# Optimization experiments

Hardware: AMD Instinct MI355X
Metric: run time of the kernel (lower is better)

Reference implementation:

```python
import jax, jax.numpy as jnp
import numpy as np

B, F, M, N, H, O = 8, 128, 256, 1024, 64, 128
BN_EPS = 1e-5
COS_EPS = 1e-8


def _bn(x, g, b, m, v):
    # inference-mode BatchNorm over channel axis 1
    shape = [1] * x.ndim
    shape[1] = -1
    return g.reshape(shape) * (x - m.reshape(shape)) * jax.lax.rsqrt(v.reshape(shape) + BN_EPS) + b.reshape(shape)


def setup_inputs() -> dict:
    key = jax.random.key(0)
    ks = jax.random.split(key, 24)
    def n(k, shape, s=1.0):
        return jax.random.normal(k, shape, dtype=jnp.float32) * s
    inp = {}
    inp['template_feature'] = n(ks[0], (B, F, M))
    inp['search_feature'] = n(ks[1], (B, F, N))
    # SharedMLP 1x1 conv weights (bias=False because bn=True)
    inp['W1'] = n(ks[2], (H, F + 1), 0.05)
    inp['W2'] = n(ks[3], (H, H), 0.05)
    inp['W3'] = n(ks[4], (H, H), 0.05)
    # fea_layer: conv1d(H, bn=True) then conv1d(O, activation=None, bias=True)
    inp['Wc1'] = n(ks[5], (H, H), 0.05)
    inp['Wc2'] = n(ks[6], (O, H), 0.05)
    inp['bc2'] = n(ks[7], (O,), 0.05)
    for i, nm in enumerate(['1', '2', '3', 'c1']):
        inp['g' + nm] = 1.0 + n(ks[8 + i], (H,), 0.1)
        inp['b' + nm] = n(ks[12 + i], (H,), 0.1)
        inp['m' + nm] = n(ks[16 + i], (H,), 0.01)
        inp['v' + nm] = jax.random.uniform(ks[20 + i], (H,), minval=0.5, maxval=1.5, dtype=jnp.float32)
    return inp


def reference(template_feature, search_feature, W1, W2, W3, Wc1, Wc2, bc2,
              g1, b1, m1, v1, g2, b2, m2, v2, g3, b3, m3, v3, gc1, bc1, mc1, vc1):
    t, s = template_feature, search_feature
    # pairwise cosine similarity over channel dim (no BxFxMxN expand needed)
    dot = jnp.einsum('bfm,bfn->bmn', t, s)
    nt = jnp.linalg.norm(t, axis=1)  # (B, M)
    ns = jnp.linalg.norm(s, axis=1)  # (B, N)
    cos = dot / jnp.maximum(nt[:, :, None] * ns[:, None, :], COS_EPS)  # (B, M, N)
    # first 1x1 conv on concat(cos, expand(t)) computed fused (no concat materialization)
    h = jnp.einsum('hf,bfm->bhm', W1[:, 1:], t)[..., None] + W1[:, 0][None, :, None, None] * cos[:, None]
    h = jax.nn.relu(_bn(h, g1, b1, m1, v1))  # (B, H, M, N)
    h = jax.nn.relu(_bn(jnp.einsum('gh,bhmn->bgmn', W2, h), g2, b2, m2, v2))
    h = jax.nn.relu(_bn(jnp.einsum('gh,bhmn->bgmn', W3, h), g3, b3, m3, v3))
    p = jnp.max(h, axis=2)  # max-pool over M -> (B, H, N)
    c = jax.nn.relu(_bn(jnp.einsum('gh,bhn->bgn', Wc1, p), gc1, bc1, mc1, vc1))
    return jnp.einsum('oh,bhn->bon', Wc2, c) + bc2[None, :, None]  # (B, O, N)
```

## Files before the change

### kernel.cpp

```cpp
#include <hip/hip_runtime.h>


#define BB 8
#define FF 128
#define MM 256
#define NN 1024
#define HH 64
#define OO 128
#define BN_EPS 1e-5f
#define COS_EPS 1e-8f

#define WS_U     0
#define WS_C2    64
#define WS_C3    128
#define WS_CC1   192
#define WS_W2F   256
#define WS_W3F   4352
#define WS_WC1F  8448
#define WS_A1    12544
#define WS_NT    143616
#define WS_NS    145664
#define WS_COSH  153856
#define WS_P     1202432
#define PS       524288

typedef _Float16 half2v __attribute__((ext_vector_type(2)));
typedef _Float16 half8  __attribute__((ext_vector_type(8)));
typedef __attribute__((ext_vector_type(4))) float f32x4;

__device__ __forceinline__ unsigned int pkh2(float a, float b){
  auto h = __builtin_amdgcn_cvt_pkrtz(a, b);
  return __builtin_bit_cast(unsigned int, h);
}
__device__ __forceinline__ half2v u2h(unsigned int u){
  return __builtin_bit_cast(half2v, u);
}
__device__ __forceinline__ unsigned int h2u(half2v v){
  return __builtin_bit_cast(unsigned int, v);
}
__device__ __forceinline__ unsigned int relu2(unsigned int d){
  half2v v = __builtin_elementwise_max(u2h(d), (half2v){(_Float16)0, (_Float16)0});
  return h2u(v);
}
__device__ __forceinline__ unsigned int bh1(unsigned int up, half2v c, unsigned int ap){
  half2v v = __builtin_elementwise_fma(u2h(up), c, u2h(ap));
  v = __builtin_elementwise_max(v, (half2v){(_Float16)0, (_Float16)0});
  return h2u(v);
}
__device__ __forceinline__ float dot4(float4 a, float4 b, float acc){
  acc = fmaf(a.x, b.x, acc); acc = fmaf(a.y, b.y, acc);
  acc = fmaf(a.z, b.z, acc); acc = fmaf(a.w, b.w, acc);
  return acc;
}

__global__ __launch_bounds__(256) void k_prep(const float* t_, const float* s_,
    const float* W1, const float* W2, const float* W3, const float* Wc1,
    const float* g1, const float* b1, const float* m1, const float* v1,
    const float* g2, const float* b2, const float* m2, const float* v2,
    const float* g3, const float* b3, const float* m3, const float* v3,
    const float* gc1,const float* bc1,const float* mc1,const float* vc1,
    float* ws){
  __shared__ float W1s[64][133];
  int t = threadIdx.x;
  int bx = blockIdx.x;
  if (bx < 256){
    int b = bx >> 5, m0 = (bx & 31)*8;
    for (int idx = t; idx < 8192; idx += 256){
      int h = idx >> 7, f = idx & 127;
      W1s[h][f] = W1[h*129 + 1 + f];
    }
    __syncthreads();
    int h = t & 63, mg = t >> 6;
    const float* tp = t_ + (size_t)b*FF*MM + m0 + mg*2;
    float acc0 = 0.f, acc1 = 0.f;
    for (int f = 0; f < FF; f++){
      float wv = W1s[h][f];
      float2 tv = *(const float2*)&tp[(size_t)f*MM];
      acc0 = fmaf(wv, tv.x, acc0); acc1 = fmaf(wv, tv.y, acc1);
    }
    float a1 = g1[h] / sqrtf(v1[h] + BN_EPS);
    float c1 = b1[h] - a1*m1[h];
    unsigned short* dst = (unsigned short*)(ws + WS_A1) + ((size_t)(b*MM + m0 + mg*2))*64 + h;
    dst[0]  = (unsigned short)(pkh2(fmaf(a1, acc0, c1), 0.f) & 0xFFFFu);
    dst[64] = (unsigned short)(pkh2(fmaf(a1, acc1, c1), 0.f) & 0xFFFFu);
  } else if (bx < 416){
    __shared__ float red[4][64];
    int x = t & 63, fq = t >> 6;
    int idx = (bx - 256)*64 + x;
    const float* ptr; size_t stride;
    if (idx < BB*MM){
      int b = idx >> 8, m = idx & 255;
      ptr = t_ + (size_t)b*FF*MM + m; stride = MM;
    } else {
      int j = idx - BB*MM;
      int b = j >> 10, n = j & 1023;
      ptr = s_ + (size_t)b*FF*NN + n; stride = NN;
    }
    float acc = 0.f;
    for (int f = fq*32; f < fq*32 + 32; f++){
      float v = ptr[(size_t)f*stride]; acc = fmaf(v, v, acc);
    }
    red[fq][x] = acc;
    __syncthreads();
    if (fq == 0)
      ws[WS_NT + idx] = sqrtf(red[0][x] + red[1][x] + red[2][x] + red[3][x]);
  } else {
    if (t < 64){
      float a1 = g1[t] / sqrtf(v1[t] + BN_EPS);
      ws[WS_U + t]   = a1 * W1[t*129];
      float a2 = g2[t] / sqrtf(v2[t] + BN_EPS);
      ws[WS_C2 + t]  = b2[t] - a2*m2[t];
      float a3 = g3[t] / sqrtf(v3[t] + BN_EPS);
      ws[WS_C3 + t]  = b3[t] - a3*m3[t];
      float ac = gc1[t] / sqrtf(vc1[t] + BN_EPS);
      ws[WS_CC1 + t] = bc1[t] - ac*mc1[t];
    }
    for (int i = t; i < 4096; i += 256){
      int g = i >> 6;
      float a2 = g2[g] / sqrtf(v2[g] + BN_EPS);
      ws[WS_W2F + i]  = a2 * W2[i];
      float a3 = g3[g] / sqrtf(v3[g] + BN_EPS);
      ws[WS_W3F + i]  = a3 * W3[i];
      float ac = gc1[g] / sqrtf(vc1[g] + BN_EPS);
      ws[WS_WC1F + i] = ac * Wc1[i];
    }
  }
}

__global__ __launch_bounds__(256) void k_cos(const float* t_, const float* s_, float* ws){
  __shared__ __align__(16) unsigned short tS[64][136];
  __shared__ __align__(16) unsigned short sS[64][136];
  __shared__ float ntS[64], nsS[64];
  int t = threadIdx.x;
  int lane = t & 63, w = t >> 6;
  int ln15 = lane & 15, quad = lane >> 4;
  int m0 = blockIdx.x*64, n0 = blockIdx.y*64, b = blockIdx.z;
  {
    int x = t & 63;
    const float* tb = t_ + (size_t)b*FF*MM + m0 + x;
    const float* sb = s_ + (size_t)b*FF*NN + n0 + x;
    #pragma unroll
    for (int k = 0; k < 16; k++){
      int fp = w*16 + k;
      *(unsigned int*)&tS[x][2*fp] = pkh2(tb[(size_t)(2*fp)*MM], tb[(size_t)(2*fp+1)*MM]);
      *(unsigned int*)&sS[x][2*fp] = pkh2(sb[(size_t)(2*fp)*NN], sb[(size_t)(2*fp+1)*NN]);
    }
    if (t < 64) ntS[t] = ws[WS_NT + b*MM + m0 + t];
    else if (t < 128) nsS[t-64] = ws[WS_NS + b*NN + n0 + (t-64)];
  }
  __syncthreads();
  half8 A4[4];
  #pragma unroll
  for (int kc = 0; kc < 4; kc++)
    A4[kc] = *(const half8*)&tS[w*16 + ln15][kc*32 + quad*8];
  float4 nt4 = *(const float4*)&ntS[w*16 + quad*4];
  unsigned short* cosw = (unsigned short*)(ws + WS_COSH);
  #pragma unroll
  for (int ns = 0; ns < 4; ns++){
    f32x4 acc = (f32x4){0.f,0.f,0.f,0.f};
    #pragma unroll
    for (int kc = 0; kc < 4; kc++){
      half8 B4 = *(const half8*)&sS[ns*16 + ln15][kc*32 + quad*8];
      acc = __builtin_amdgcn_mfma_f32_16x16x32_f16(A4[kc], B4, acc, 0, 0, 0);
    }
    float nsv = nsS[ns*16 + ln15];
    int n = n0 + ns*16 + ln15;
    #pragma unroll
    for (int r = 0; r < 4; r++){
      int m = m0 + w*16 + quad*4 + r;
      float denom = fmaxf(nt4[r]*nsv, COS_EPS);
      float c = acc[r] * __builtin_amdgcn_rcpf(denom);
      cosw[(size_t)(b*MM + m)*NN + n] = (unsigned short)(pkh2(c, 0.f) & 0xFFFFu);
    }
  }
}

__global__ __launch_bounds__(256, 3) void k_main(const float* ws, float* Pp){
  __shared__ __align__(16) unsigned short h2W[4][16][72];
  int t = threadIdx.x;
  int lane = t & 63, w = t >> 6;
  int ln15 = lane & 15, quad = lane >> 4;
  int b = blockIdx.y;
  int n0 = blockIdx.x * 32;
  int ms = blockIdx.z;

  const float* w2p = ws + WS_W2F;
  const float* w3p = ws + WS_W3F;
  half8 W2A[4][2], W3A[4][2];
  f32x4 c2v[4], c3v[4];
  #pragma unroll
  for (int rt = 0; rt < 4; rt++){
    int g = rt*16 + ln15;
    #pragma unroll
    for (int kk = 0; kk < 2; kk++){
      half8 a2, a3;
      #pragma unroll
      for (int j = 0; j < 8; j++){
        int k = kk*32 + quad*8 + j;
        a2[j] = (_Float16)w2p[g*64 + k];
        a3[j] = (_Float16)w3p[g*64 + k];
      }
      W2A[rt][kk] = a2; W3A[rt][kk] = a3;
    }
    float4 cb2 = *(const float4*)&ws[WS_C2 + rt*16 + quad*4];
    float4 cb3 = *(const float4*)&ws[WS_C3 + rt*16 + quad*4];
    c2v[rt] = (f32x4){cb2.x, cb2.y, cb2.z, cb2.w};
    c3v[rt] = (f32x4){cb3.x, cb3.y, cb3.z, cb3.w};
  }
  unsigned int upk[2][4];
  #pragma unroll
  for (int kk = 0; kk < 2; kk++){
    float4 ua = *(const float4*)&ws[WS_U + kk*32 + quad*8];
    float4 ub = *(const float4*)&ws[WS_U + kk*32 + quad*8 + 4];
    upk[kk][0] = pkh2(ua.x, ua.y); upk[kk][1] = pkh2(ua.z, ua.w);
    upk[kk][2] = pkh2(ub.x, ub.y); upk[kk][3] = pkh2(ub.z, ub.w);
  }
  const unsigned short* A1H = (const unsigned short*)(ws + WS_A1) + (size_t)b*MM*64;
  int mp = w >> 1;
  int n  = n0 + (w & 1)*16 + ln15;
  const unsigned short* cosP = (const unsigned short*)(ws + WS_COSH)
                               + (size_t)b*MM*NN + n;
  unsigned short* h2w = &h2W[w][0][0];

  f32x4 p[4];
  #pragma unroll
  for (int rt = 0; rt < 4; rt++) p[rt] = (f32x4){0.f,0.f,0.f,0.f};

  int m0i = ms*128 + mp;
  unsigned int cu = cosP[(size_t)m0i*NN];
  uint4 a1a = *(const uint4*)&A1H[(size_t)m0i*64 + quad*8];
  uint4 a1b = *(const uint4*)&A1H[(size_t)m0i*64 + 32 + quad*8];

  for (int mc = 0; mc < 64; mc++){
    int mN = ms*128 + (mc < 63 ? (mc + 1) : 63)*2 + mp;
    unsigned int cuN = cosP[(size_t)mN*NN];
    uint4 a1aN = *(const uint4*)&A1H[(size_t)mN*64 + quad*8];
    uint4 a1bN = *(const uint4*)&A1H[(size_t)mN*64 + 32 + quad*8];

    unsigned int cd = cu | (cu << 16);
    half2v ch = u2h(cd);
    uint4 q0, q1;
    q0.x = bh1(upk[0][0], ch, a1a.x); q0.y = bh1(upk[0][1], ch, a1a.y);
    q0.z = bh1(upk[0][2], ch, a1a.z); q0.w = bh1(upk[0][3], ch, a1a.w);
    q1.x = bh1(upk[1][0], ch, a1b.x); q1.y = bh1(upk[1][1], ch, a1b.y);
    q1.z = bh1(upk[1][2], ch, a1b.z); q1.w = bh1(upk[1][3], ch, a1b.w);
    half8 b0h = __builtin_bit_cast(half8, q0);
    half8 b1h = __builtin_bit_cast(half8, q1);

    f32x4 acc[4];
    #pragma unroll
    for (int rt = 0; rt < 4; rt++){
      acc[rt] = __builtin_amdgcn_mfma_f32_16x16x32_f16(W2A[rt][0], b0h, c2v[rt], 0, 0, 0);
      acc[rt] = __builtin_amdgcn_mfma_f32_16x16x32_f16(W2A[rt][1], b1h, acc[rt], 0, 0, 0);
    }
    #pragma unroll
    for (int rt = 0; rt < 4; rt++){
      uint2 vv;
      vv.x = relu2(pkh2(acc[rt][0], acc[rt][1]));
      vv.y = relu2(pkh2(acc[rt][2], acc[rt][3]));
      *(uint2*)&h2w[ln15*72 + rt*16 + quad*4] = vv;
    }
    __asm__ volatile("s_waitcnt lgkmcnt(0)" ::: "memory");
    half8 e0 = *(const half8*)&h2w[ln15*72 + quad*8];
    half8 e1 = *(const half8*)&h2w[ln15*72 + 32 + quad*8];
    #pragma unroll
    for (int rt = 0; rt < 4; rt++){
      f32x4 a3 = __builtin_amdgcn_mfma_f32_16x16x32_f16(W3A[rt][0], e0, c3v[rt], 0, 0, 0);
      a3 = __builtin_amdgcn_mfma_f32_16x16x32_f16(W3A[rt][1], e1, a3, 0, 0, 0);
      #pragma unroll
      for (int r = 0; r < 4; r++) p[rt][r] = fmaxf(p[rt][r], a3[r]);
    }
    cu = cuN; a1a = a1aN; a1b = a1bN;
  }

  __syncthreads();
  float* redBuf = (float*)&h2W[0][0][0];
  if (w >= 2){
    #pragma unroll
    for (int rt = 0; rt < 4; rt++){
      f32x4 v = p[rt];
      *(float4*)&redBuf[(size_t)(((w & 1)*16 + ln15)*66 + rt*16 + quad*4)] =
          make_float4(v[0], v[1], v[2], v[3]);
    }
  }
  __syncthreads();
  if (w < 2){
    float* Pb = Pp + (size_t)ms*PS + ((size_t)(b*NN + n) << 6);
    #pragma unroll
    for (int rt = 0; rt < 4; rt++){
      float4 o = *(const float4*)&redBuf[(size_t)(((w & 1)*16 + ln15)*66 + rt*16 + quad*4)];
      float4 r4;
      r4.x = fmaxf(p[rt][0], o.x);
      r4.y = fmaxf(p[rt][1], o.y);
      r4.z = fmaxf(p[rt][2], o.z);
      r4.w = fmaxf(p[rt][3], o.w);
      *(float4*)&Pb[rt*16 + quad*4] = r4;
    }
  }
}

__global__ __launch_bounds__(256) void k_tail(const float* Wc2, const float* bc2,
                                              const float* ws, float* out){
  __shared__ float WT[64][68];
  __shared__ float pT[32][68];
  __shared__ float cS[32][68];
  int t = threadIdx.x;
  int n0 = blockIdx.x * 32;
  int b = blockIdx.y;
  for (int i = t; i < 4096; i += 256) WT[i >> 6][i & 63] = ws[WS_WC1F + i];
  const float* P0 = ws + WS_P + ((size_t)(b*NN + n0) << 6);
  const float* P1 = P0 + PS;
  for (int i = t; i < 2048; i += 256) pT[i >> 6][i & 63] = fmaxf(P0[i], P1[i]);
  __syncthreads();
  {
    int n = t & 31, q = t >> 5;
    for (int k = 0; k < 8; k++){
      int g = q*8 + k;
      float acc = ws[WS_CC1 + g];
      for (int hs = 0; hs < 64; hs += 4){
        float4 wv = *(const float4*)&WT[g][hs];
        float4 pv = *(const float4*)&pT[n][hs];
        acc = dot4(wv, pv, acc);
      }
      cS[n][g] = fmaxf(acc, 0.f);
    }
  }
  __syncthreads();
  {
    int o = t & 127, hf = t >> 7;
    float bco = bc2[o];
    float accO[16];
    #pragma unroll
    for (int i = 0; i < 16; i++) accO[i] = bco;
    for (int hs = 0; hs < 64; hs += 4){
      float4 w4 = *(const float4*)&Wc2[o*64 + hs];
      #pragma unroll
      for (int i = 0; i < 16; i++){
        float4 cv = *(const float4*)&cS[hf*16 + i][hs];
        accO[i] = dot4(w4, cv, accO[i]);
      }
    }
    #pragma unroll
    for (int i = 0; i < 16; i++)
      out[((size_t)(b*OO + o))*NN + n0 + hf*16 + i] = accO[i];
  }
}

extern "C" void kernel_launch(void* const* d_in, const int* in_sizes, int n_in,
                              void* d_out, int out_size, void* d_ws, size_t ws_size,
                              hipStream_t stream){
  (void)in_sizes; (void)n_in; (void)out_size; (void)ws_size;
  const float* t_  = (const float*)d_in[0];
  const float* s_  = (const float*)d_in[1];
  const float* W1  = (const float*)d_in[2];
  const float* W2  = (const float*)d_in[3];
  const float* W3  = (const float*)d_in[4];
  const float* Wc1 = (const float*)d_in[5];
  const float* Wc2 = (const float*)d_in[6];
  const float* bc2 = (const float*)d_in[7];
  const float* g1 = (const float*)d_in[8],  *b1 = (const float*)d_in[9],
             * m1 = (const float*)d_in[10], *v1 = (const float*)d_in[11];
  const float* g2 = (const float*)d_in[12], *b2 = (const float*)d_in[13],
             * m2 = (const float*)d_in[14], *v2 = (const float*)d_in[15];
  const float* g3 = (const float*)d_in[16], *b3 = (const float*)d_in[17],
             * m3 = (const float*)d_in[18], *v3 = (const float*)d_in[19];
  const float* gc1 = (const float*)d_in[20], *bc1 = (const float*)d_in[21],
             * mc1 = (const float*)d_in[22], *vc1 = (const float*)d_in[23];
  float* ws = (float*)d_ws;
  float* out = (float*)d_out;

  k_prep<<<417, 256, 0, stream>>>(t_, s_, W1, W2, W3, Wc1,
      g1,b1,m1,v1, g2,b2,m2,v2, g3,b3,m3,v3, gc1,bc1,mc1,vc1, ws);
  k_cos<<<dim3(4, 16, 8), 256, 0, stream>>>(t_, s_, ws);
  k_main<<<dim3(32, 8, 2), 256, 0, stream>>>(ws, ws + WS_P);
  k_tail<<<dim3(32, 8), 256, 0, stream>>>(Wc2, bc2, ws, out);
}
```

Before: 188.0 us.

## Fuse cosine similarity and norms into main kernel, split M into four slices

Removes the separate norm and cosine kernels. Each main block now loads its 64x128 template tile and 32x128 search tile, computes the norms and the fp16 cosine tile into shared memory with MFMA, then runs the MLP over its 64 M rows. This drops the global round trip of the 8x256x1024 fp16 cosine matrix and one kernel launch. The grid doubles to four M slices, and the layer-3 bias and ReLU are moved after the max-pool. The main loop is unrolled by two M rows and occupancy is raised to 4 waves. In exchange, search features are reloaded and their norms recomputed by each of the four M-slice blocks, and the tail reduces over four partials.

```diff
diff --git a/kernel.cpp b/kernel.cpp
--- a/kernel.cpp
+++ b/kernel.cpp
@@ -18,10 +18,7 @@
 #define WS_W3F   4352
 #define WS_WC1F  8448
 #define WS_A1    12544
-#define WS_NT    143616
-#define WS_NS    145664
-#define WS_COSH  153856
-#define WS_P     1202432
+#define WS_P     78080
 #define PS       524288
 
 typedef _Float16 half2v __attribute__((ext_vector_type(2)));
@@ -53,7 +50,7 @@
   return acc;
 }
 
-__global__ __launch_bounds__(256) void k_prep(const float* t_, const float* s_,
+__global__ __launch_bounds__(256) void k_prep(const float* t_,
     const float* W1, const float* W2, const float* W3, const float* Wc1,
     const float* g1, const float* b1, const float* m1, const float* v1,
     const float* g2, const float* b2, const float* m2, const float* v2,
@@ -83,27 +80,6 @@
     unsigned short* dst = (unsigned short*)(ws + WS_A1) + ((size_t)(b*MM + m0 + mg*2))*64 + h;
     dst[0]  = (unsigned short)(pkh2(fmaf(a1, acc0, c1), 0.f) & 0xFFFFu);
     dst[64] = (unsigned short)(pkh2(fmaf(a1, acc1, c1), 0.f) & 0xFFFFu);
-  } else if (bx < 416){
-    __shared__ float red[4][64];
-    int x = t & 63, fq = t >> 6;
-    int idx = (bx - 256)*64 + x;
-    const float* ptr; size_t stride;
-    if (idx < BB*MM){
-      int b = idx >> 8, m = idx & 255;
-      ptr = t_ + (size_t)b*FF*MM + m; stride = MM;
-    } else {
-      int j = idx - BB*MM;
-      int b = j >> 10, n = j & 1023;
-      ptr = s_ + (size_t)b*FF*NN + n; stride = NN;
-    }
-    float acc = 0.f;
-    for (int f = fq*32; f < fq*32 + 32; f++){
-      float v = ptr[(size_t)f*stride]; acc = fmaf(v, v, acc);
-    }
-    red[fq][x] = acc;
-    __syncthreads();
-    if (fq == 0)
-      ws[WS_NT + idx] = sqrtf(red[0][x] + red[1][x] + red[2][x] + red[3][x]);
   } else {
     if (t < 64){
       float a1 = g1[t] / sqrtf(v1[t] + BN_EPS);
@@ -127,67 +103,86 @@
   }
 }
 
-__global__ __launch_bounds__(256) void k_cos(const float* t_, const float* s_, float* ws){
-  __shared__ __align__(16) unsigned short tS[64][136];
-  __shared__ __align__(16) unsigned short sS[64][136];
-  __shared__ float ntS[64], nsS[64];
-  int t = threadIdx.x;
-  int lane = t & 63, w = t >> 6;
-  int ln15 = lane & 15, quad = lane >> 4;
-  int m0 = blockIdx.x*64, n0 = blockIdx.y*64, b = blockIdx.z;
-  {
-    int x = t & 63;
-    const float* tb = t_ + (size_t)b*FF*MM + m0 + x;
-    const float* sb = s_ + (size_t)b*FF*NN + n0 + x;
-    #pragma unroll
-    for (int k = 0; k < 16; k++){
-      int fp = w*16 + k;
-      *(unsigned int*)&tS[x][2*fp] = pkh2(tb[(size_t)(2*fp)*MM], tb[(size_t)(2*fp+1)*MM]);
-      *(unsigned int*)&sS[x][2*fp] = pkh2(sb[(size_t)(2*fp)*NN], sb[(size_t)(2*fp+1)*NN]);
-    }
-    if (t < 64) ntS[t] = ws[WS_NT + b*MM + m0 + t];
-    else if (t < 128) nsS[t-64] = ws[WS_NS + b*NN + n0 + (t-64)];
-  }
-  __syncthreads();
-  half8 A4[4];
-  #pragma unroll
-  for (int kc = 0; kc < 4; kc++)
-    A4[kc] = *(const half8*)&tS[w*16 + ln15][kc*32 + quad*8];
-  float4 nt4 = *(const float4*)&ntS[w*16 + quad*4];
-  unsigned short* cosw = (unsigned short*)(ws + WS_COSH);
-  #pragma unroll
-  for (int ns = 0; ns < 4; ns++){
-    f32x4 acc = (f32x4){0.f,0.f,0.f,0.f};
-    #pragma unroll
-    for (int kc = 0; kc < 4; kc++){
-      half8 B4 = *(const half8*)&sS[ns*16 + ln15][kc*32 + quad*8];
-      acc = __builtin_amdgcn_mfma_f32_16x16x32_f16(A4[kc], B4, acc, 0, 0, 0);
-    }
-    float nsv = nsS[ns*16 + ln15];
-    int n = n0 + ns*16 + ln15;
-    #pragma unroll
-    for (int r = 0; r < 4; r++){
-      int m = m0 + w*16 + quad*4 + r;
-      float denom = fmaxf(nt4[r]*nsv, COS_EPS);
-      float c = acc[r] * __builtin_amdgcn_rcpf(denom);
-      cosw[(size_t)(b*MM + m)*NN + n] = (unsigned short)(pkh2(c, 0.f) & 0xFFFFu);
-    }
-  }
-}
-
-__global__ __launch_bounds__(256, 3) void k_main(const float* ws, float* Pp){
-  __shared__ __align__(16) unsigned short h2W[4][16][72];
+__global__ __launch_bounds__(256, 4) void k_main(const float* t_, const float* s_,
+                                                 const float* ws, float* Pp){
+  __shared__ __align__(16) char smem[32896];
+  unsigned short* cosL = (unsigned short*)smem;
+  float* ntF = (float*)(smem + 4352);
+  float* nsF = (float*)(smem + 4608);
+  unsigned short* tT = (unsigned short*)(smem + 4736);
+  unsigned short* sT = (unsigned short*)(smem + 22144);
+  float* redT = (float*)(smem + 30848);
+  float* redS = (float*)(smem + 31872);
+  unsigned short* h2base = (unsigned short*)(smem + 4736);
+
   int t = threadIdx.x;
   int lane = t & 63, w = t >> 6;
   int ln15 = lane & 15, quad = lane >> 4;
   int b = blockIdx.y;
   int n0 = blockIdx.x * 32;
-  int ms = blockIdx.z;
+  int m0 = blockIdx.z * 64;
+
+  {
+    int fg = t >> 6;
+    const float* tb = t_ + ((size_t)(b*FF + fg*32))*MM + m0 + lane;
+    float accT = 0.f;
+    #pragma unroll
+    for (int k = 0; k < 16; k++){
+      float va = tb[(size_t)(2*k)*MM], vb = tb[(size_t)(2*k+1)*MM];
+      accT = fmaf(va, va, accT); accT = fmaf(vb, vb, accT);
+      *(unsigned int*)&tT[lane*136 + fg*32 + 2*k] = pkh2(va, vb);
+    }
+    redT[fg*64 + lane] = accT;
+    int n = t & 31, fg2 = t >> 5;
+    const float* sb = s_ + ((size_t)(b*FF + fg2*16))*NN + n0 + n;
+    float accS = 0.f;
+    #pragma unroll
+    for (int k = 0; k < 8; k++){
+      float va = sb[(size_t)(2*k)*NN], vb = sb[(size_t)(2*k+1)*NN];
+      accS = fmaf(va, va, accS); accS = fmaf(vb, vb, accS);
+      *(unsigned int*)&sT[n*136 + fg2*16 + 2*k] = pkh2(va, vb);
+    }
+    redS[fg2*32 + n] = accS;
+  }
+  __syncthreads();
+  if (t < 64){
+    ntF[t] = sqrtf(redT[t] + redT[64+t] + redT[128+t] + redT[192+t]);
+  } else if (t < 96){
+    int n = t - 64;
+    float s = redS[n] + redS[32+n] + redS[64+n] + redS[96+n]
+            + redS[128+n] + redS[160+n] + redS[192+n] + redS[224+n];
+    nsF[n] = sqrtf(s);
+  }
+  __syncthreads();
+  {
+    half8 At[4];
+    #pragma unroll
+    for (int kc = 0; kc < 4; kc++)
+      At[kc] = *(const half8*)&tT[(w*16 + ln15)*136 + kc*32 + quad*8];
+    float4 ntv = *(const float4*)&ntF[w*16 + quad*4];
+    #pragma unroll
+    for (int nt2 = 0; nt2 < 2; nt2++){
+      f32x4 acc = (f32x4){0.f,0.f,0.f,0.f};
+      #pragma unroll
+      for (int kc = 0; kc < 4; kc++){
+        half8 Bs = *(const half8*)&sT[(nt2*16 + ln15)*136 + kc*32 + quad*8];
+        acc = __builtin_amdgcn_mfma_f32_16x16x32_f16(At[kc], Bs, acc, 0, 0, 0);
+      }
+      float nsv = nsF[nt2*16 + ln15];
+      #pragma unroll
+      for (int r = 0; r < 4; r++){
+        float denom = fmaxf(ntv[r == 0 ? 0 : (r == 1 ? 1 : (r == 2 ? 2 : 3))] * nsv, COS_EPS);
+        float c = acc[r] * __builtin_amdgcn_rcpf(denom);
+        cosL[(w*16 + quad*4 + r)*34 + nt2*16 + ln15] = (unsigned short)(pkh2(c, 0.f) & 0xFFFFu);
+      }
+    }
+  }
+  __syncthreads();
 
   const float* w2p = ws + WS_W2F;
   const float* w3p = ws + WS_W3F;
   half8 W2A[4][2], W3A[4][2];
-  f32x4 c2v[4], c3v[4];
+  f32x4 c2v[4];
   #pragma unroll
   for (int rt = 0; rt < 4; rt++){
     int g = rt*16 + ln15;
@@ -203,9 +198,7 @@
       W2A[rt][kk] = a2; W3A[rt][kk] = a3;
     }
     float4 cb2 = *(const float4*)&ws[WS_C2 + rt*16 + quad*4];
-    float4 cb3 = *(const float4*)&ws[WS_C3 + rt*16 + quad*4];
     c2v[rt] = (f32x4){cb2.x, cb2.y, cb2.z, cb2.w};
-    c3v[rt] = (f32x4){cb3.x, cb3.y, cb3.z, cb3.w};
   }
   unsigned int upk[2][4];
   #pragma unroll
@@ -217,83 +210,126 @@
   }
   const unsigned short* A1H = (const unsigned short*)(ws + WS_A1) + (size_t)b*MM*64;
   int mp = w >> 1;
-  int n  = n0 + (w & 1)*16 + ln15;
-  const unsigned short* cosP = (const unsigned short*)(ws + WS_COSH)
-                               + (size_t)b*MM*NN + n;
-  unsigned short* h2w = &h2W[w][0][0];
+  int nl = (w & 1)*16 + ln15;
+  int n  = n0 + nl;
+  unsigned short* h2w = h2base + w*2304;
 
   f32x4 p[4];
   #pragma unroll
-  for (int rt = 0; rt < 4; rt++) p[rt] = (f32x4){0.f,0.f,0.f,0.f};
-
-  int m0i = ms*128 + mp;
-  unsigned int cu = cosP[(size_t)m0i*NN];
-  uint4 a1a = *(const uint4*)&A1H[(size_t)m0i*64 + quad*8];
-  uint4 a1b = *(const uint4*)&A1H[(size_t)m0i*64 + 32 + quad*8];
-
-  for (int mc = 0; mc < 64; mc++){
-    int mN = ms*128 + (mc < 63 ? (mc + 1) : 63)*2 + mp;
-    unsigned int cuN = cosP[(size_t)mN*NN];
-    uint4 a1aN = *(const uint4*)&A1H[(size_t)mN*64 + quad*8];
-    uint4 a1bN = *(const uint4*)&A1H[(size_t)mN*64 + 32 + quad*8];
-
-    unsigned int cd = cu | (cu << 16);
-    half2v ch = u2h(cd);
-    uint4 q0, q1;
-    q0.x = bh1(upk[0][0], ch, a1a.x); q0.y = bh1(upk[0][1], ch, a1a.y);
-    q0.z = bh1(upk[0][2], ch, a1a.z); q0.w = bh1(upk[0][3], ch, a1a.w);
-    q1.x = bh1(upk[1][0], ch, a1b.x); q1.y = bh1(upk[1][1], ch, a1b.y);
-    q1.z = bh1(upk[1][2], ch, a1b.z); q1.w = bh1(upk[1][3], ch, a1b.w);
-    half8 b0h = __builtin_bit_cast(half8, q0);
-    half8 b1h = __builtin_bit_cast(half8, q1);
-
-    f32x4 acc[4];
-    #pragma unroll
-    for (int rt = 0; rt < 4; rt++){
-      acc[rt] = __builtin_amdgcn_mfma_f32_16x16x32_f16(W2A[rt][0], b0h, c2v[rt], 0, 0, 0);
-      acc[rt] = __builtin_amdgcn_mfma_f32_16x16x32_f16(W2A[rt][1], b1h, acc[rt], 0, 0, 0);
-    }
-    #pragma unroll
-    for (int rt = 0; rt < 4; rt++){
-      uint2 vv;
-      vv.x = relu2(pkh2(acc[rt][0], acc[rt][1]));
-      vv.y = relu2(pkh2(acc[rt][2], acc[rt][3]));
-      *(uint2*)&h2w[ln15*72 + rt*16 + quad*4] = vv;
-    }
+  for (int rt = 0; rt < 4; rt++) p[rt] = (f32x4){-3e38f, -3e38f, -3e38f, -3e38f};
+  const f32x4 ZER4 = (f32x4){0.f,0.f,0.f,0.f};
+
+  uint4 aAa = *(const uint4*)&A1H[(size_t)(m0 + 0*2 + mp)*64 + quad*8];
+  uint4 aAb = *(const uint4*)&A1H[(size_t)(m0 + 0*2 + mp)*64 + 32 + quad*8];
+  uint4 aBa = *(const uint4*)&A1H[(size_t)(m0 + 1*2 + mp)*64 + quad*8];
+  uint4 aBb = *(const uint4*)&A1H[(size_t)(m0 + 1*2 + mp)*64 + 32 + quad*8];
+  unsigned int cuA = cosL[(0*2 + mp)*34 + nl];
+  unsigned int cuB = cosL[(1*2 + mp)*34 + nl];
+
+  for (int i = 0; i < 32; i += 2){
+    {
+      unsigned int cd = cuA | (cuA << 16);
+      half2v ch = u2h(cd);
+      uint4 q0, q1;
+      q0.x = bh1(upk[0][0], ch, aAa.x); q0.y = bh1(upk[0][1], ch, aAa.y);
+      q0.z = bh1(upk[0][2], ch, aAa.z); q0.w = bh1(upk[0][3], ch, aAa.w);
+      q1.x = bh1(upk[1][0], ch, aAb.x); q1.y = bh1(upk[1][1], ch, aAb.y);
+      q1.z = bh1(upk[1][2], ch, aAb.z); q1.w = bh1(upk[1][3], ch, aAb.w);
+      half8 b0h = __builtin_bit_cast(half8, q0);
+      half8 b1h = __builtin_bit_cast(half8, q1);
+      f32x4 acc[4];
+      #pragma unroll
+      for (int rt = 0; rt < 4; rt++){
+        acc[rt] = __builtin_amdgcn_mfma_f32_16x16x32_f16(W2A[rt][0], b0h, c2v[rt], 0, 0, 0);
+        acc[rt] = __builtin_amdgcn_mfma_f32_16x16x32_f16(W2A[rt][1], b1h, acc[rt], 0, 0, 0);
+      }
+      #pragma unroll
+      for (int rt = 0; rt < 4; rt++){
+        uint2 vv;
+        vv.x = relu2(pkh2(acc[rt][0], acc[rt][1]));
+        vv.y = relu2(pkh2(acc[rt][2], acc[rt][3]));
+        *(uint2*)&h2w[ln15*72 + rt*16 + quad*4] = vv;
+      }
+    }
+    {
+      unsigned int cd = cuB | (cuB << 16);
+      half2v ch = u2h(cd);
+      uint4 q0, q1;
+      q0.x = bh1(upk[0][0], ch, aBa.x); q0.y = bh1(upk[0][1], ch, aBa.y);
+      q0.z = bh1(upk[0][2], ch, aBa.z); q0.w = bh1(upk[0][3], ch, aBa.w);
+      q1.x = bh1(upk[1][0], ch, aBb.x); q1.y = bh1(upk[1][1], ch, aBb.y);
+      q1.z = bh1(upk[1][2], ch, aBb.z); q1.w = bh1(upk[1][3], ch, aBb.w);
+      half8 b0h = __builtin_bit_cast(half8, q0);
+      half8 b1h = __builtin_bit_cast(half8, q1);
+      f32x4 acc[4];
+      #pragma unroll
+      for (int rt = 0; rt < 4; rt++){
+        acc[rt] = __builtin_amdgcn_mfma_f32_16x16x32_f16(W2A[rt][0], b0h, c2v[rt], 0, 0, 0);
+        acc[rt] = __builtin_amdgcn_mfma_f32_16x16x32_f16(W2A[rt][1], b1h, acc[rt], 0, 0, 0);
+      }
+      #pragma unroll
+      for (int rt = 0; rt < 4; rt++){
+        uint2 vv;
+        vv.x = relu2(pkh2(acc[rt][0], acc[rt][1]));
+        vv.y = relu2(pkh2(acc[rt][2], acc[rt][3]));
+        *(uint2*)&h2w[1152 + ln15*72 + rt*16 + quad*4] = vv;
+      }
+    }
+    int i2 = (i + 2 < 32) ? i + 2 : 30;
+    int i3 = (i + 3 < 32) ? i + 3 : 31;
+    unsigned int cuA2 = cosL[(i2*2 + mp)*34 + nl];
+    unsigned int cuB2 = cosL[(i3*2 + mp)*34 + nl];
+    uint4 nAa = *(const uint4*)&A1H[(size_t)(m0 + i2*2 + mp)*64 + quad*8];
+    uint4 nAb = *(const uint4*)&A1H[(size_t)(m0 + i2*2 + mp)*64 + 32 + quad*8];
+    uint4 nBa = *(const uint4*)&A1H[(size_t)(m0 + i3*2 + mp)*64 + quad*8];
+    uint4 nBb = *(const uint4*)&A1H[(size_t)(m0 + i3*2 + mp)*64 + 32 + quad*8];
     __asm__ volatile("s_waitcnt lgkmcnt(0)" ::: "memory");
-    half8 e0 = *(const half8*)&h2w[ln15*72 + quad*8];
-    half8 e1 = *(const half8*)&h2w[ln15*72 + 32 + quad*8];
-    #pragma unroll
-    for (int rt = 0; rt < 4; rt++){
-      f32x4 a3 = __builtin_amdgcn_mfma_f32_16x16x32_f16(W3A[rt][0], e0, c3v[rt], 0, 0, 0);
-      a3 = __builtin_amdgcn_mfma_f32_16x16x32_f16(W3A[rt][1], e1, a3, 0, 0, 0);
-      #pragma unroll
-      for (int r = 0; r < 4; r++) p[rt][r] = fmaxf(p[rt][r], a3[r]);
-    }
-    cu = cuN; a1a = a1aN; a1b = a1bN;
-  }
-
-  __syncthreads();
-  float* redBuf = (float*)&h2W[0][0][0];
+    {
+      half8 e0 = *(const half8*)&h2w[ln15*72 + quad*8];
+      half8 e1 = *(const half8*)&h2w[ln15*72 + 32 + quad*8];
+      #pragma unroll
+      for (int rt = 0; rt < 4; rt++){
+        f32x4 a3 = __builtin_amdgcn_mfma_f32_16x16x32_f16(W3A[rt][0], e0, ZER4, 0, 0, 0);
+        a3 = __builtin_amdgcn_mfma_f32_16x16x32_f16(W3A[rt][1], e1, a3, 0, 0, 0);
+        #pragma unroll
+        for (int r = 0; r < 4; r++) p[rt][r] = fmaxf(p[rt][r], a3[r]);
+      }
+      half8 f0 = *(const half8*)&h2w[1152 + ln15*72 + quad*8];
+      half8 f1 = *(const half8*)&h2w[1152 + ln15*72 + 32 + quad*8];
+      #pragma unroll
+      for (int rt = 0; rt < 4; rt++){
+        f32x4 a3 = __builtin_amdgcn_mfma_f32_16x16x32_f16(W3A[rt][0], f0, ZER4, 0, 0, 0);
+        a3 = __builtin_amdgcn_mfma_f32_16x16x32_f16(W3A[rt][1], f1, a3, 0, 0, 0);
+        #pragma unroll
+        for (int r = 0; r < 4; r++) p[rt][r] = fmaxf(p[rt][r], a3[r]);
+      }
+    }
+    cuA = cuA2; cuB = cuB2;
+    aAa = nAa; aAb = nAb; aBa = nBa; aBb = nBb;
+  }
+
+  __syncthreads();
+  float* redBuf = (float*)(smem + 4736);
   if (w >= 2){
     #pragma unroll
     for (int rt = 0; rt < 4; rt++){
       f32x4 v = p[rt];
-      *(float4*)&redBuf[(size_t)(((w & 1)*16 + ln15)*66 + rt*16 + quad*4)] =
+      *(float4*)&redBuf[(size_t)((nl)*66 + rt*16 + quad*4)] =
           make_float4(v[0], v[1], v[2], v[3]);
     }
   }
   __syncthreads();
   if (w < 2){
-    float* Pb = Pp + (size_t)ms*PS + ((size_t)(b*NN + n) << 6);
+    float* Pb = Pp + (size_t)blockIdx.z*PS + ((size_t)(b*NN + n) << 6);
     #pragma unroll
     for (int rt = 0; rt < 4; rt++){
-      float4 o = *(const float4*)&redBuf[(size_t)(((w & 1)*16 + ln15)*66 + rt*16 + quad*4)];
+      float4 o = *(const float4*)&redBuf[(size_t)((nl)*66 + rt*16 + quad*4)];
+      float4 c3r = *(const float4*)&ws[WS_C3 + rt*16 + quad*4];
       float4 r4;
-      r4.x = fmaxf(p[rt][0], o.x);
-      r4.y = fmaxf(p[rt][1], o.y);
-      r4.z = fmaxf(p[rt][2], o.z);
-      r4.w = fmaxf(p[rt][3], o.w);
+      r4.x = fmaxf(fmaxf(p[rt][0], o.x) + c3r.x, 0.f);
+      r4.y = fmaxf(fmaxf(p[rt][1], o.y) + c3r.y, 0.f);
+      r4.z = fmaxf(fmaxf(p[rt][2], o.z) + c3r.z, 0.f);
+      r4.w = fmaxf(fmaxf(p[rt][3], o.w) + c3r.w, 0.f);
       *(float4*)&Pb[rt*16 + quad*4] = r4;
     }
   }
@@ -309,8 +345,10 @@
   int b = blockIdx.y;
   for (int i = t; i < 4096; i += 256) WT[i >> 6][i & 63] = ws[WS_WC1F + i];
   const float* P0 = ws + WS_P + ((size_t)(b*NN + n0) << 6);
-  const float* P1 = P0 + PS;
-  for (int i = t; i < 2048; i += 256) pT[i >> 6][i & 63] = fmaxf(P0[i], P1[i]);
+  for (int i = t; i < 2048; i += 256){
+    float v = fmaxf(fmaxf(P0[i], P0[PS + i]), fmaxf(P0[2*PS + i], P0[3*PS + i]));
+    pT[i >> 6][i & 63] = v;
+  }
   __syncthreads();
   {
     int n = t & 31, q = t >> 5;
@@ -369,9 +407,8 @@
   float* ws = (float*)d_ws;
   float* out = (float*)d_out;
 
-  k_prep<<<417, 256, 0, stream>>>(t_, s_, W1, W2, W3, Wc1,
+  k_prep<<<257, 256, 0, stream>>>(t_, W1, W2, W3, Wc1,
       g1,b1,m1,v1, g2,b2,m2,v2, g3,b3,m3,v3, gc1,bc1,mc1,vc1, ws);
-  k_cos<<<dim3(4, 16, 8), 256, 0, stream>>>(t_, s_, ws);
-  k_main<<<dim3(32, 8, 2), 256, 0, stream>>>(ws, ws + WS_P);
+  k_main<<<dim3(32, 8, 4), 256, 0, stream>>>(t_, s_, ws, ws + WS_P);
   k_tail<<<dim3(32, 8), 256, 0, stream>>>(Wc2, bc2, ws, out);
 }
```

Result: slower. 250.6 us (+33.3%).

## Restructure main loop: per-wave M slices, deferred bias/ReLU, fp16 pre-packed inputs

Applied to the files above, without the earlier changes.

The norm pass in k_prep now also writes fp16-packed copies of the template and search features, so k_cos loads half-width pre-packed data instead of converting fp32 strided loads itself. k_main now gives each wave its own M slice over 16 columns, doubling the grid, and processes two M rows per iteration through double-buffered LDS scratch. The layer-3 bias and ReLU move out of the inner loop to after the max, which is valid because both are monotonic. This removes per-iteration bias accumulation and ReLU work and raises occupancy, at the cost of an extra workspace round-trip for the packed features and a wider cross-wave reduction.

```diff
diff --git a/kernel.cpp b/kernel.cpp
--- a/kernel.cpp
+++ b/kernel.cpp
@@ -18,10 +18,12 @@
 #define WS_W3F   4352
 #define WS_WC1F  8448
 #define WS_A1    12544
-#define WS_NT    143616
-#define WS_NS    145664
-#define WS_COSH  153856
-#define WS_P     1202432
+#define WS_COSH  78080
+#define WS_TH    1126656
+#define WS_SH    1257728
+#define WS_NT    1782016
+#define WS_NS    1784064
+#define WS_P     1126656
 #define PS       524288
 
 typedef _Float16 half2v __attribute__((ext_vector_type(2)));
@@ -85,20 +87,32 @@
     dst[64] = (unsigned short)(pkh2(fmaf(a1, acc1, c1), 0.f) & 0xFFFFu);
   } else if (bx < 416){
     __shared__ float red[4][64];
+    unsigned int* thp = (unsigned int*)(ws + WS_TH);
+    unsigned int* shp = (unsigned int*)(ws + WS_SH);
     int x = t & 63, fq = t >> 6;
     int idx = (bx - 256)*64 + x;
-    const float* ptr; size_t stride;
+    float acc = 0.f;
     if (idx < BB*MM){
       int b = idx >> 8, m = idx & 255;
-      ptr = t_ + (size_t)b*FF*MM + m; stride = MM;
+      const float* ptr = t_ + (size_t)b*FF*MM + m;
+      #pragma unroll
+      for (int k = 0; k < 16; k++){
+        int f = fq*32 + 2*k;
+        float va = ptr[(size_t)f*MM], vb = ptr[(size_t)(f+1)*MM];
+        acc = fmaf(va, va, acc); acc = fmaf(vb, vb, acc);
+        thp[(size_t)(b*64 + fq*16 + k)*MM + m] = pkh2(va, vb);
+      }
     } else {
       int j = idx - BB*MM;
       int b = j >> 10, n = j & 1023;
-      ptr = s_ + (size_t)b*FF*NN + n; stride = NN;
-    }
-    float acc = 0.f;
-    for (int f = fq*32; f < fq*32 + 32; f++){
-      float v = ptr[(size_t)f*stride]; acc = fmaf(v, v, acc);
+      const float* ptr = s_ + (size_t)b*FF*NN + n;
+      #pragma unroll
+      for (int k = 0; k < 16; k++){
+        int f = fq*32 + 2*k;
+        float va = ptr[(size_t)f*NN], vb = ptr[(size_t)(f+1)*NN];
+        acc = fmaf(va, va, acc); acc = fmaf(vb, vb, acc);
+        shp[(size_t)(b*64 + fq*16 + k)*NN + n] = pkh2(va, vb);
+      }
     }
     red[fq][x] = acc;
     __syncthreads();
@@ -127,7 +141,7 @@
   }
 }
 
-__global__ __launch_bounds__(256) void k_cos(const float* t_, const float* s_, float* ws){
+__global__ __launch_bounds__(256) void k_cos(float* ws){
   __shared__ __align__(16) unsigned short tS[64][136];
   __shared__ __align__(16) unsigned short sS[64][136];
   __shared__ float ntS[64], nsS[64];
@@ -136,14 +150,12 @@
   int ln15 = lane & 15, quad = lane >> 4;
   int m0 = blockIdx.x*64, n0 = blockIdx.y*64, b = blockIdx.z;
   {
-    int x = t & 63;
-    const float* tb = t_ + (size_t)b*FF*MM + m0 + x;
-    const float* sb = s_ + (size_t)b*FF*NN + n0 + x;
-    #pragma unroll
-    for (int k = 0; k < 16; k++){
-      int fp = w*16 + k;
-      *(unsigned int*)&tS[x][2*fp] = pkh2(tb[(size_t)(2*fp)*MM], tb[(size_t)(2*fp+1)*MM]);
-      *(unsigned int*)&sS[x][2*fp] = pkh2(sb[(size_t)(2*fp)*NN], sb[(size_t)(2*fp+1)*NN]);
+    const unsigned int* thp = (const unsigned int*)(ws + WS_TH);
+    const unsigned int* shp = (const unsigned int*)(ws + WS_SH);
+    for (int i = t; i < 4096; i += 256){
+      int x = i & 63, fp = i >> 6;
+      *(unsigned int*)&tS[x][2*fp] = thp[(size_t)(b*64 + fp)*MM + m0 + x];
+      *(unsigned int*)&sS[x][2*fp] = shp[(size_t)(b*64 + fp)*NN + n0 + x];
     }
     if (t < 64) ntS[t] = ws[WS_NT + b*MM + m0 + t];
     else if (t < 128) nsS[t-64] = ws[WS_NS + b*NN + n0 + (t-64)];
@@ -175,19 +187,19 @@
   }
 }
 
-__global__ __launch_bounds__(256, 3) void k_main(const float* ws, float* Pp){
-  __shared__ __align__(16) unsigned short h2W[4][16][72];
+__global__ __launch_bounds__(256, 4) void k_main(const float* ws, float* Pp){
+  __shared__ __align__(16) unsigned short h2W[4][2][16][72];
   int t = threadIdx.x;
   int lane = t & 63, w = t >> 6;
   int ln15 = lane & 15, quad = lane >> 4;
   int b = blockIdx.y;
-  int n0 = blockIdx.x * 32;
+  int n0 = blockIdx.x * 16;
   int ms = blockIdx.z;
 
   const float* w2p = ws + WS_W2F;
   const float* w3p = ws + WS_W3F;
   half8 W2A[4][2], W3A[4][2];
-  f32x4 c2v[4], c3v[4];
+  f32x4 c2v[4];
   #pragma unroll
   for (int rt = 0; rt < 4; rt++){
     int g = rt*16 + ln15;
@@ -203,9 +215,7 @@
       W2A[rt][kk] = a2; W3A[rt][kk] = a3;
     }
     float4 cb2 = *(const float4*)&ws[WS_C2 + rt*16 + quad*4];
-    float4 cb3 = *(const float4*)&ws[WS_C3 + rt*16 + quad*4];
     c2v[rt] = (f32x4){cb2.x, cb2.y, cb2.z, cb2.w};
-    c3v[rt] = (f32x4){cb3.x, cb3.y, cb3.z, cb3.w};
   }
   unsigned int upk[2][4];
   #pragma unroll
@@ -216,84 +226,134 @@
     upk[kk][2] = pkh2(ub.x, ub.y); upk[kk][3] = pkh2(ub.z, ub.w);
   }
   const unsigned short* A1H = (const unsigned short*)(ws + WS_A1) + (size_t)b*MM*64;
-  int mp = w >> 1;
-  int n  = n0 + (w & 1)*16 + ln15;
-  const unsigned short* cosP = (const unsigned short*)(ws + WS_COSH)
-                               + (size_t)b*MM*NN + n;
-  unsigned short* h2w = &h2W[w][0][0];
+  int n = n0 + ln15;
+  const unsigned short* cosP = (const unsigned short*)(ws + WS_COSH) + (size_t)b*MM*NN + n;
+  unsigned short* h2w0 = &h2W[w][0][0][0];
+  unsigned short* h2w1 = &h2W[w][1][0][0];
 
   f32x4 p[4];
   #pragma unroll
-  for (int rt = 0; rt < 4; rt++) p[rt] = (f32x4){0.f,0.f,0.f,0.f};
-
-  int m0i = ms*128 + mp;
-  unsigned int cu = cosP[(size_t)m0i*NN];
-  uint4 a1a = *(const uint4*)&A1H[(size_t)m0i*64 + quad*8];
-  uint4 a1b = *(const uint4*)&A1H[(size_t)m0i*64 + 32 + quad*8];
-
-  for (int mc = 0; mc < 64; mc++){
-    int mN = ms*128 + (mc < 63 ? (mc + 1) : 63)*2 + mp;
-    unsigned int cuN = cosP[(size_t)mN*NN];
-    uint4 a1aN = *(const uint4*)&A1H[(size_t)mN*64 + quad*8];
-    uint4 a1bN = *(const uint4*)&A1H[(size_t)mN*64 + 32 + quad*8];
-
-    unsigned int cd = cu | (cu << 16);
-    half2v ch = u2h(cd);
-    uint4 q0, q1;
-    q0.x = bh1(upk[0][0], ch, a1a.x); q0.y = bh1(upk[0][1], ch, a1a.y);
-    q0.z = bh1(upk[0][2], ch, a1a.z); q0.w = bh1(upk[0][3], ch, a1a.w);
-    q1.x = bh1(upk[1][0], ch, a1b.x); q1.y = bh1(upk[1][1], ch, a1b.y);
-    q1.z = bh1(upk[1][2], ch, a1b.z); q1.w = bh1(upk[1][3], ch, a1b.w);
-    half8 b0h = __builtin_bit_cast(half8, q0);
-    half8 b1h = __builtin_bit_cast(half8, q1);
-
-    f32x4 acc[4];
-    #pragma unroll
-    for (int rt = 0; rt < 4; rt++){
-      acc[rt] = __builtin_amdgcn_mfma_f32_16x16x32_f16(W2A[rt][0], b0h, c2v[rt], 0, 0, 0);
-      acc[rt] = __builtin_amdgcn_mfma_f32_16x16x32_f16(W2A[rt][1], b1h, acc[rt], 0, 0, 0);
-    }
-    #pragma unroll
-    for (int rt = 0; rt < 4; rt++){
-      uint2 vv;
-      vv.x = relu2(pkh2(acc[rt][0], acc[rt][1]));
-      vv.y = relu2(pkh2(acc[rt][2], acc[rt][3]));
-      *(uint2*)&h2w[ln15*72 + rt*16 + quad*4] = vv;
-    }
+  for (int rt = 0; rt < 4; rt++) p[rt] = (f32x4){-3e38f, -3e38f, -3e38f, -3e38f};
+  const f32x4 ZER4 = (f32x4){0.f,0.f,0.f,0.f};
+
+  int mA = ms*128 + 0*4 + w;
+  int mB = ms*128 + 1*4 + w;
+  unsigned int cuA = cosP[(size_t)mA*NN];
+  unsigned int cuB = cosP[(size_t)mB*NN];
+  uint4 aAa = *(const uint4*)&A1H[(size_t)mA*64 + quad*8];
+  uint4 aAb = *(const uint4*)&A1H[(size_t)mA*64 + 32 + quad*8];
+  uint4 aBa = *(const uint4*)&A1H[(size_t)mB*64 + quad*8];
+  uint4 aBb = *(const uint4*)&A1H[(size_t)mB*64 + 32 + quad*8];
+
+  for (int j = 0; j < 32; j += 2){
+    {
+      unsigned int cd = cuA | (cuA << 16);
+      half2v ch = u2h(cd);
+      uint4 q0, q1;
+      q0.x = bh1(upk[0][0], ch, aAa.x); q0.y = bh1(upk[0][1], ch, aAa.y);
+      q0.z = bh1(upk[0][2], ch, aAa.z); q0.w = bh1(upk[0][3], ch, aAa.w);
+      q1.x = bh1(upk[1][0], ch, aAb.x); q1.y = bh1(upk[1][1], ch, aAb.y);
+      q1.z = bh1(upk[1][2], ch, aAb.z); q1.w = bh1(upk[1][3], ch, aAb.w);
+      half8 b0h = __builtin_bit_cast(half8, q0);
+      half8 b1h = __builtin_bit_cast(half8, q1);
+      f32x4 acc[4];
+      #pragma unroll
+      for (int rt = 0; rt < 4; rt++){
+        acc[rt] = __builtin_amdgcn_mfma_f32_16x16x32_f16(W2A[rt][0], b0h, c2v[rt], 0, 0, 0);
+        acc[rt] = __builtin_amdgcn_mfma_f32_16x16x32_f16(W2A[rt][1], b1h, acc[rt], 0, 0, 0);
+      }
+      #pragma unroll
+      for (int rt = 0; rt < 4; rt++){
+        uint2 vv;
+        vv.x = relu2(pkh2(acc[rt][0], acc[rt][1]));
+        vv.y = relu2(pkh2(acc[rt][2], acc[rt][3]));
+        *(uint2*)&h2w0[ln15*72 + rt*16 + quad*4] = vv;
+      }
+    }
+    {
+      unsigned int cd = cuB | (cuB << 16);
+      half2v ch = u2h(cd);
+      uint4 q0, q1;
+      q0.x = bh1(upk[0][0], ch, aBa.x); q0.y = bh1(upk[0][1], ch, aBa.y);
+      q0.z = bh1(upk[0][2], ch, aBa.z); q0.w = bh1(upk[0][3], ch, aBa.w);
+      q1.x = bh1(upk[1][0], ch, aBb.x); q1.y = bh1(upk[1][1], ch, aBb.y);
+      q1.z = bh1(upk[1][2], ch, aBb.z); q1.w = bh1(upk[1][3], ch, aBb.w);
+      half8 b0h = __builtin_bit_cast(half8, q0);
+      half8 b1h = __builtin_bit_cast(half8, q1);
+      f32x4 acc[4];
+      #pragma unroll
+      for (int rt = 0; rt < 4; rt++){
+        acc[rt] = __builtin_amdgcn_mfma_f32_16x16x32_f16(W2A[rt][0], b0h, c2v[rt], 0, 0, 0);
+        acc[rt] = __builtin_amdgcn_mfma_f32_16x16x32_f16(W2A[rt][1], b1h, acc[rt], 0, 0, 0);
+      }
+      #pragma unroll
+      for (int rt = 0; rt < 4; rt++){
+        uint2 vv;
+        vv.x = relu2(pkh2(acc[rt][0], acc[rt][1]));
+        vv.y = relu2(pkh2(acc[rt][2], acc[rt][3]));
+        *(uint2*)&h2w1[ln15*72 + rt*16 + quad*4] = vv;
+      }
+    }
+    int j2 = (j + 2 < 32) ? j + 2 : 30;
+    int j3 = (j + 3 < 32) ? j + 3 : 31;
+    int m2i = ms*128 + j2*4 + w;
+    int m3i = ms*128 + j3*4 + w;
+    unsigned int cuA2 = cosP[(size_t)m2i*NN];
+    unsigned int cuB2 = cosP[(size_t)m3i*NN];
+    uint4 nAa = *(const uint4*)&A1H[(size_t)m2i*64 + quad*8];
+    uint4 nAb = *(const uint4*)&A1H[(size_t)m2i*64 + 32 + quad*8];
+    uint4 nBa = *(const uint4*)&A1H[(size_t)m3i*64 + quad*8];
+    uint4 nBb = *(const uint4*)&A1H[(size_t)m3i*64 + 32 + quad*8];
     __asm__ volatile("s_waitcnt lgkmcnt(0)" ::: "memory");
-    half8 e0 = *(const half8*)&h2w[ln15*72 + quad*8];
-    half8 e1 = *(const half8*)&h2w[ln15*72 + 32 + quad*8];
-    #pragma unroll
-    for (int rt = 0; rt < 4; rt++){
-      f32x4 a3 = __builtin_amdgcn_mfma_f32_16x16x32_f16(W3A[rt][0], e0, c3v[rt], 0, 0, 0);
-      a3 = __builtin_amdgcn_mfma_f32_16x16x32_f16(W3A[rt][1], e1, a3, 0, 0, 0);
-      #pragma unroll
-      for (int r = 0; r < 4; r++) p[rt][r] = fmaxf(p[rt][r], a3[r]);
-    }
-    cu = cuN; a1a = a1aN; a1b = a1bN;
+    {
+      half8 e0 = *(const half8*)&h2w0[ln15*72 + quad*8];
+      half8 e1 = *(const half8*)&h2w0[ln15*72 + 32 + quad*8];
+      #pragma unroll
+      for (int rt = 0; rt < 4; rt++){
+        f32x4 a3 = __builtin_amdgcn_mfma_f32_16x16x32_f16(W3A[rt][0], e0, ZER4, 0, 0, 0);
+        a3 = __builtin_amdgcn_mfma_f32_16x16x32_f16(W3A[rt][1], e1, a3, 0, 0, 0);
+        #pragma unroll
+        for (int r = 0; r < 4; r++) p[rt][r] = fmaxf(p[rt][r], a3[r]);
+      }
+      half8 f0 = *(const half8*)&h2w1[ln15*72 + quad*8];
+      half8 f1 = *(const half8*)&h2w1[ln15*72 + 32 + quad*8];
+      #pragma unroll
+      for (int rt = 0; rt < 4; rt++){
+        f32x4 a3 = __builtin_amdgcn_mfma_f32_16x16x32_f16(W3A[rt][0], f0, ZER4, 0, 0, 0);
+        a3 = __builtin_amdgcn_mfma_f32_16x16x32_f16(W3A[rt][1], f1, a3, 0, 0, 0);
+        #pragma unroll
+        for (int r = 0; r < 4; r++) p[rt][r] = fmaxf(p[rt][r], a3[r]);
+      }
+    }
+    cuA = cuA2; cuB = cuB2;
+    aAa = nAa; aAb = nAb; aBa = nBa; aBb = nBb;
   }
 
   __syncthreads();
-  float* redBuf = (float*)&h2W[0][0][0];
-  if (w >= 2){
+  float* redBuf = (float*)&h2W[0][0][0][0];
+  if (w >= 1){
     #pragma unroll
     for (int rt = 0; rt < 4; rt++){
       f32x4 v = p[rt];
-      *(float4*)&redBuf[(size_t)(((w & 1)*16 + ln15)*66 + rt*16 + quad*4)] =
+      *(float4*)&redBuf[(size_t)((w-1)*1088 + ln15*68 + rt*16 + quad*4)] =
           make_float4(v[0], v[1], v[2], v[3]);
     }
   }
   __syncthreads();
-  if (w < 2){
+  if (w == 0){
     float* Pb = Pp + (size_t)ms*PS + ((size_t)(b*NN + n) << 6);
     #pragma unroll
     for (int rt = 0; rt < 4; rt++){
-      float4 o = *(const float4*)&redBuf[(size_t)(((w & 1)*16 + ln15)*66 + rt*16 + quad*4)];
+      int off = ln15*68 + rt*16 + quad*4;
+      float4 o1 = *(const float4*)&redBuf[off];
+      float4 o2 = *(const float4*)&redBuf[1088 + off];
+      float4 o3 = *(const float4*)&redBuf[2176 + off];
+      float4 c3r = *(const float4*)&ws[WS_C3 + rt*16 + quad*4];
       float4 r4;
-      r4.x = fmaxf(p[rt][0], o.x);
-      r4.y = fmaxf(p[rt][1], o.y);
-      r4.z = fmaxf(p[rt][2], o.z);
-      r4.w = fmaxf(p[rt][3], o.w);
+      r4.x = fmaxf(fmaxf(fmaxf(p[rt][0], o1.x), fmaxf(o2.x, o3.x)) + c3r.x, 0.f);
+      r4.y = fmaxf(fmaxf(fmaxf(p[rt][1], o1.y), fmaxf(o2.y, o3.y)) + c3r.y, 0.f);
+      r4.z = fmaxf(fmaxf(fmaxf(p[rt][2], o1.z), fmaxf(o2.z, o3.z)) + c3r.z, 0.f);
+      r4.w = fmaxf(fmaxf(fmaxf(p[rt][3], o1.w), fmaxf(o2.w, o3.w)) + c3r.w, 0.f);
       *(float4*)&Pb[rt*16 + quad*4] = r4;
     }
   }
@@ -371,7 +431,7 @@
 
   k_prep<<<417, 256, 0, stream>>>(t_, s_, W1, W2, W3, Wc1,
       g1,b1,m1,v1, g2,b2,m2,v2, g3,b3,m3,v3, gc1,bc1,mc1,vc1, ws);
-  k_cos<<<dim3(4, 16, 8), 256, 0, stream>>>(t_, s_, ws);
-  k_main<<<dim3(32, 8, 2), 256, 0, stream>>>(ws, ws + WS_P);
+  k_cos<<<dim3(4, 16, 8), 256, 0, stream>>>(ws);
+  k_main<<<dim3(64, 8, 2), 256, 0, stream>>>(ws, ws + WS_P);
   k_tail<<<dim3(32, 8), 256, 0, stream>>>(Wc2, bc2, ws, out);
 }
```

Result: slower. 251.4 us (+33.7%).
